# Optimization experiments

Measured on AMD Instinct MI355X. Metric: run time of the kernel, lower is better.

## Reference

```python
import jax, jax.numpy as jnp
import numpy as np

IMG = 1536
STRIDES = [8, 16, 32, 64, 128]
SCALES = np.array([2.0 ** 0, 2.0 ** (1.0 / 3.0), 2.0 ** (2.0 / 3.0)])
RATIOS = np.array([0.5, 1.0, 2.0])
THRESHOLD = 0.5
IOU_THRESHOLD = 0.5
N_KEEP = 1000  # fixed candidate budget for jit-compatible NMS


def make_anchors():
    """Multi-level RetinaNet-style anchors in (x1, y1, x2, y2), [A, 4]."""
    all_boxes = []
    for s in STRIDES:
        base = 4.0 * s
        fs = IMG // s
        areas = (base * SCALES) ** 2
        ws, hs = [], []
        for r in RATIOS:
            ws.append(np.sqrt(areas / r))
            hs.append(np.sqrt(areas * r))
        ws = np.concatenate(ws)  # [9]
        hs = np.concatenate(hs)
        cx = (np.arange(fs) + 0.5) * s
        cy = (np.arange(fs) + 0.5) * s
        cxg, cyg = np.meshgrid(cx, cy)
        cxg = cxg.reshape(-1, 1)
        cyg = cyg.reshape(-1, 1)
        boxes = np.stack([cxg - ws / 2, cyg - hs / 2, cxg + ws / 2, cyg + hs / 2], axis=-1)
        all_boxes.append(boxes.reshape(-1, 4))
    return np.concatenate(all_boxes, axis=0).astype(np.float32)


def setup_inputs() -> dict:
    key = jax.random.key(0)
    k1, k2 = jax.random.split(key)
    anchors = jnp.asarray(make_anchors())  # [441936, 4]
    A = anchors.shape[0]
    cla = jax.random.uniform(k1, (1, A, 80), dtype=jnp.float32)  # sigmoid-like class scores
    reg = 0.1 * jax.random.normal(k2, (1, A, 4), dtype=jnp.float32)  # box deltas
    return {"cla": cla, "reg": reg, "anchors": anchors, "height": IMG, "width": IMG}


def decode_box(anchors, deltas):
    wa = anchors[:, 2] - anchors[:, 0]
    ha = anchors[:, 3] - anchors[:, 1]
    cxa = anchors[:, 0] + 0.5 * wa
    cya = anchors[:, 1] + 0.5 * ha
    cx = cxa + deltas[:, 0] * wa
    cy = cya + deltas[:, 1] * ha
    w = wa * jnp.exp(deltas[:, 2])
    h = ha * jnp.exp(deltas[:, 3])
    return jnp.stack([cx - 0.5 * w, cy - 0.5 * h, cx + 0.5 * w, cy + 0.5 * h], axis=-1)


def iou_matrix(b):
    x1 = jnp.maximum(b[:, None, 0], b[None, :, 0])
    y1 = jnp.maximum(b[:, None, 1], b[None, :, 1])
    x2 = jnp.minimum(b[:, None, 2], b[None, :, 2])
    y2 = jnp.minimum(b[:, None, 3], b[None, :, 3])
    inter = jnp.clip(x2 - x1, 0.0) * jnp.clip(y2 - y1, 0.0)
    area = jnp.clip(b[:, 2] - b[:, 0], 0.0) * jnp.clip(b[:, 3] - b[:, 1], 0.0)
    union = area[:, None] + area[None, :] - inter
    return inter / jnp.maximum(union, 1e-8)


def reference(cla, reg, anchors, height, width):
    # decode + clip (clipbox)
    boxes = decode_box(anchors, reg[0])  # [A, 4]
    boxes = jnp.stack([
        jnp.clip(boxes[:, 0], 0.0, width - 1.0),
        jnp.clip(boxes[:, 1], 0.0, height - 1.0),
        jnp.clip(boxes[:, 2], 0.0, width - 1.0),
        jnp.clip(boxes[:, 3], 0.0, height - 1.0),
    ], axis=-1)
    # per-anchor best class score (torch.max over dim=2)
    scores_all = jnp.max(cla[0], axis=1)  # [A]
    # fixed-size candidate set replaces data-dependent boolean masking
    top_scores, idx = jax.lax.top_k(scores_all, N_KEEP)
    cand_boxes = boxes[idx]            # [N, 4]
    cand_cla = cla[0][idx]             # [N, C]
    valid = top_scores > THRESHOLD     # score thresholding
    iou = iou_matrix(cand_boxes)       # [N, N]

    def body(i, keep):
        suppressed = jnp.any(keep & (iou[i] > IOU_THRESHOLD))
        return keep.at[i].set(valid[i] & ~suppressed)

    keep = jax.lax.fori_loop(0, N_KEEP, body, jnp.zeros((N_KEEP,), dtype=bool))

    nms_scores = jnp.where(keep, jnp.max(cand_cla, axis=1), 0.0)
    nms_class = jnp.where(keep, jnp.argmax(cand_cla, axis=1), -1)
    nms_boxes = jnp.where(keep[:, None], cand_boxes, 0.0)
    return nms_scores, nms_class, nms_boxes
```

## Files before the change

kernel.cpp:

```cpp
#include <hip/hip_runtime.h>
#include <stdint.h>


#define NK 1000
#define CAP 2048
#define NCLS 80
#define NW 16
typedef unsigned long long ull;

static inline __device__ unsigned fkey(float f) {
  unsigned u = __float_as_uint(f);
  return (u & 0x80000000u) ? ~u : (u | 0x80000000u);
}
static inline __device__ float fkey_inv(unsigned k) {
  unsigned u = (k & 0x80000000u) ? (k & 0x7fffffffu) : ~k;
  return __uint_as_float(u);
}

__device__ __forceinline__ void scan_select(const unsigned* __restrict__ gh, int nbins,
                                            unsigned k, unsigned* s_sum, unsigned* s_res,
                                            unsigned& digit, unsigned& cum_above) {
  int t = threadIdx.x;
  int chunk = nbins >> 8;
  if (chunk < 1) chunk = 1;
  int base = t * chunk;
  unsigned s = 0;
  for (int b = 0; b < chunk; ++b) s += gh[base + b];
  s_sum[t] = s;
  __syncthreads();
  unsigned ca = 0;
  for (int u = t + 1; u < 256; ++u) ca += s_sum[u];
  if (ca < k && ca + s >= k) {
    unsigned cum = ca;
    for (int b = chunk - 1; b >= 0; --b) {
      unsigned c = gh[base + b];
      if (cum + c >= k) { s_res[0] = (unsigned)(base + b); s_res[1] = cum; break; }
      cum += c;
    }
  }
  __syncthreads();
  digit = s_res[0];
  cum_above = s_res[1];
  __syncthreads();
}

__global__ __launch_bounds__(256) void k_score(const float* __restrict__ cla,
                                               unsigned* __restrict__ keys,
                                               unsigned* __restrict__ hist0,
                                               uint4* __restrict__ zreg, int nz4,
                                               int A) {
  __shared__ unsigned lh[4096];
  int t = threadIdx.x;
  {
    const uint4 z = make_uint4(0u, 0u, 0u, 0u);
    int stride = gridDim.x * 256;
    for (int i = blockIdx.x * 256 + t; i < nz4; i += stride) zreg[i] = z;
  }
  for (int i = t; i < 4096; i += 256) lh[i] = 0u;
  __syncthreads();
  const int lane = t & 63, wib = t >> 6;
  const int gwave = blockIdx.x * 4 + wib, nwaves = gridDim.x * 4;
  const int q = lane >> 2, sub = lane & 3;
  const int ntask = (A + 15) >> 4;
  for (int task = gwave; task < ntask; task += nwaves) {
    int a = task * 16 + q;
    float m = -3.402823466e38f;
    if (a < A) {
      const float4* p = (const float4*)(cla + (size_t)a * NCLS);
#pragma unroll
      for (int j = 0; j < 5; ++j) {
        float4 v = p[sub + j * 4];
        m = fmaxf(m, fmaxf(fmaxf(v.x, v.y), fmaxf(v.z, v.w)));
      }
    }
    m = fmaxf(m, __shfl_xor(m, 1, 64));
    m = fmaxf(m, __shfl_xor(m, 2, 64));
    if (sub == 0 && a < A) {
      unsigned key = fkey(m);
      keys[a] = key;
      atomicAdd(&lh[key >> 20], 1u);
    }
  }
  __syncthreads();
  for (int i = t; i < 4096; i += 256) {
    unsigned c = lh[i];
    if (c) atomicAdd(&hist0[i], c);
  }
}

__global__ __launch_bounds__(256) void k_hist1(const unsigned* __restrict__ keys,
                                               const unsigned* __restrict__ hist0,
                                               unsigned* __restrict__ leaf,
                                               unsigned* __restrict__ summary, int A) {
  __shared__ unsigned lh[4096];
  __shared__ unsigned s_sum[256];
  __shared__ unsigned s_res[2];
  int t = threadIdx.x;
  unsigned d0, ca;
  scan_select(hist0, 4096, NK, s_sum, s_res, d0, ca);
  for (int i = t; i < 4096; i += 256) lh[i] = 0u;
  __syncthreads();
  int tid = blockIdx.x * 256 + t, nthr = gridDim.x * 256;
  for (int a = tid; a < A; a += nthr) {
    unsigned key = keys[a];
    if ((key >> 20) == d0) {
      unsigned low = key & 0xFFFFFu;
      atomicAdd(&leaf[low], 1u);
      atomicAdd(&lh[low >> 8], 1u);
    }
  }
  __syncthreads();
  for (int i = t; i < 4096; i += 256) {
    unsigned c = lh[i];
    if (c) atomicAdd(&summary[i], c);
  }
}

__global__ __launch_bounds__(256) void k_gather(const unsigned* __restrict__ keys,
                                                const unsigned* __restrict__ hist0,
                                                const unsigned* __restrict__ leaf,
                                                const unsigned* __restrict__ summary,
                                                unsigned* __restrict__ meta,
                                                ull* __restrict__ cand_keys, int A) {
  __shared__ unsigned s_sum[256];
  __shared__ unsigned s_res[2];
  __shared__ ull lbuf[1024];
  __shared__ unsigned lcnt;
  __shared__ unsigned gbase;
  int t = threadIdx.x;
  unsigned k_rem = NK, d0, g, b, ca;
  scan_select(hist0, 4096, k_rem, s_sum, s_res, d0, ca);
  k_rem -= ca;
  scan_select(summary, 4096, k_rem, s_sum, s_res, g, ca);
  k_rem -= ca;
  scan_select(leaf + (size_t)g * 256, 256, k_rem, s_sum, s_res, b, ca);
  const unsigned T = (d0 << 20) | (g << 8) | b;
  if (t == 0) lcnt = 0u;
  __syncthreads();
  int tid = blockIdx.x * 256 + t, nthr = gridDim.x * 256;
  for (int a = tid; a < A; a += nthr) {
    unsigned key = keys[a];
    if (key >= T) {
      unsigned pos = atomicAdd(&lcnt, 1u);
      if (pos < 1024)
        lbuf[pos] = ((ull)key << 32) | (ull)(~(unsigned)a);
    }
  }
  __syncthreads();
  if (t == 0) gbase = (lcnt > 0) ? atomicAdd(&meta[0], lcnt) : 0u;
  __syncthreads();
  unsigned n = lcnt < 1024u ? lcnt : 1024u;
  for (unsigned i = t; i < n; i += 256) {
    unsigned pos = gbase + i;
    if (pos < CAP) cand_keys[pos] = lbuf[i];
  }
}

__global__ __launch_bounds__(256) void k_rankdec(
    const float* __restrict__ cla, const float* __restrict__ reg,
    const float* __restrict__ anchors, const int* __restrict__ hp,
    const int* __restrict__ wp, const ull* __restrict__ cand_keys,
    float4* __restrict__ cand_box, float* __restrict__ cand_area,
    float* __restrict__ cand_score, int* __restrict__ cand_cls,
    int* __restrict__ cand_valid) {
  __shared__ ull skeys[CAP];
  int t = threadIdx.x;
  for (int i = t; i < CAP; i += 256) skeys[i] = cand_keys[i];
  __syncthreads();
  int c = blockIdx.x * 256 + t;
  ull ck = skeys[c];
  if (ck == 0ull) return;
  unsigned cnt = 0;
  const ulonglong2* sk2 = (const ulonglong2*)skeys;
#pragma unroll 4
  for (int j = 0; j < CAP / 2; ++j) {
    ulonglong2 v = sk2[j];
    cnt += (v.x > ck) ? 1u : 0u;
    cnt += (v.y > ck) ? 1u : 0u;
  }
  if (cnt >= NK) return;
  int rank = (int)cnt;
  unsigned a = ~(unsigned)(ck & 0xFFFFFFFFull);
  float score = fkey_inv((unsigned)(ck >> 32));
  float W1 = (float)wp[0] - 1.0f;
  float H1 = (float)hp[0] - 1.0f;
  float4 dd = ((const float4*)reg)[a];
  float4 an = ((const float4*)anchors)[a];
  float wa = an.z - an.x, ha = an.w - an.y;
  float cxa = an.x + 0.5f * wa, cya = an.y + 0.5f * ha;
  float cx = cxa + dd.x * wa, cy = cya + dd.y * ha;
  float w = wa * expf(dd.z), h = ha * expf(dd.w);
  float x1 = fminf(fmaxf(cx - 0.5f * w, 0.0f), W1);
  float y1 = fminf(fmaxf(cy - 0.5f * h, 0.0f), H1);
  float x2 = fminf(fmaxf(cx + 0.5f * w, 0.0f), W1);
  float y2 = fminf(fmaxf(cy + 0.5f * h, 0.0f), H1);
  cand_box[rank] = make_float4(x1, y1, x2, y2);
  cand_area[rank] = fmaxf(x2 - x1, 0.0f) * fmaxf(y2 - y1, 0.0f);
  cand_score[rank] = score;
  cand_valid[rank] = (score > 0.5f) ? 1 : 0;
  const float* row = cla + (size_t)a * NCLS;
  float m = -3.402823466e38f;
  int ci = 0;
#pragma unroll
  for (int j = 0; j < NCLS; ++j) {
    float v = row[j];
    if (v > m) { m = v; ci = j; }
  }
  cand_cls[rank] = ci;
}

__global__ __launch_bounds__(256) void k_supres(const float4* __restrict__ cand_box,
                                                const float* __restrict__ cand_area,
                                                const int* __restrict__ cand_valid,
                                                const float* __restrict__ cand_score,
                                                const int* __restrict__ cand_cls,
                                                ull* __restrict__ sup,
                                                unsigned* __restrict__ meta,
                                                float* __restrict__ out) {
  __shared__ float4 bx[NK];
  __shared__ float ar[NK];
  __shared__ ull keep_sh[NW];
  __shared__ int s_last;
  int t = threadIdx.x;
  for (int i = t; i < NK; i += 256) {
    bx[i] = cand_box[i];
    ar[i] = cand_area[i];
  }
  __syncthreads();
  int gidx = blockIdx.x * 256 + t;
  int i = gidx >> 4, w = gidx & 15;
  if (i < NK) {
    float4 bi = bx[i];
    float ai = ar[i];
    ull bits = 0ull;
    int j0 = w * 64;
    int jend = (j0 + 64 < NK) ? (j0 + 64) : NK;
    for (int j = j0; j < jend; ++j) {
      float4 bj = bx[j];
      float xx1 = fmaxf(bi.x, bj.x), yy1 = fmaxf(bi.y, bj.y);
      float xx2 = fminf(bi.z, bj.z), yy2 = fminf(bi.w, bj.w);
      float inter = fmaxf(xx2 - xx1, 0.0f) * fmaxf(yy2 - yy1, 0.0f);
      float uni = ai + ar[j] - inter;
      float iou = inter / fmaxf(uni, 1e-8f);
      if (iou > 0.5f) bits |= (1ull << (j - j0));
    }
    sup[(size_t)i * NW + w] = bits;
  }
  __threadfence();
  __syncthreads();
  if (t == 0) {
    unsigned done = __hip_atomic_fetch_add(&meta[1], 1u, __ATOMIC_ACQ_REL,
                                           __HIP_MEMORY_SCOPE_AGENT);
    s_last = (done == gridDim.x - 1) ? 1 : 0;
  }
  __syncthreads();
  if (!s_last) return;
  __threadfence();
  if (t < 64) {
    int lane = t;
    ull keepw[NW];
#pragma unroll
    for (int c = 0; c < NW; ++c) {
      int row = c * 64 + lane;
      ull rw[NW];
      int vld = 0;
      if (row < NK) {
#pragma unroll
        for (int w2 = 0; w2 < NW; ++w2)
          rw[w2] = __hip_atomic_load(&sup[(size_t)row * NW + w2], __ATOMIC_RELAXED,
                                     __HIP_MEMORY_SCOPE_AGENT);
        vld = cand_valid[row];
      } else {
#pragma unroll
        for (int w2 = 0; w2 < NW; ++w2) rw[w2] = 0ull;
      }
      ull prev = 0ull;
#pragma unroll
      for (int w2 = 0; w2 < NW; ++w2)
        if (w2 < c) prev |= rw[w2] & keepw[w2];
      int flags = (vld ? 2 : 0) | ((prev != 0ull) ? 1 : 0);
      unsigned Llo = (unsigned)rw[c];
      unsigned Lhi = (unsigned)(rw[c] >> 32);
      ull kept = 0ull;
      for (int b = 0; b < 64; ++b) {
        int fb = __shfl(flags, b, 64);
        unsigned lo = (unsigned)__shfl((int)Llo, b, 64);
        unsigned hi = (unsigned)__shfl((int)Lhi, b, 64);
        ull Lb = ((ull)hi << 32) | (ull)lo;
        bool kp = ((fb & 2) != 0) && ((fb & 1) == 0) && ((Lb & kept) == 0ull);
        kept |= ((ull)(kp ? 1u : 0u)) << b;
      }
      keepw[c] = kept;
    }
    if (lane == 0) {
#pragma unroll
      for (int w2 = 0; w2 < NW; ++w2) keep_sh[w2] = keepw[w2];
    }
  }
  __syncthreads();
  for (int i2 = t; i2 < NK; i2 += 256) {
    bool kp = (keep_sh[i2 >> 6] >> (i2 & 63)) & 1ull;
    out[i2] = kp ? cand_score[i2] : 0.0f;
    out[NK + i2] = kp ? (float)cand_cls[i2] : -1.0f;
    float4 bo = cand_box[i2];
    ((float4*)(out + 2 * NK))[i2] = kp ? bo : make_float4(0.f, 0.f, 0.f, 0.f);
  }
}

extern "C" void kernel_launch(void* const* d_in, const int* in_sizes, int n_in,
                              void* d_out, int out_size, void* d_ws, size_t ws_size,
                              hipStream_t stream) {
  const float* cla = (const float*)d_in[0];
  const float* reg = (const float*)d_in[1];
  const float* anchors = (const float*)d_in[2];
  const int* hp = (const int*)d_in[3];
  const int* wp = (const int*)d_in[4];
  float* out = (float*)d_out;
  int A = in_sizes[2] / 4;

  char* ws = (char*)d_ws;
  size_t off = 0;
  auto carve = [&](size_t bytes) -> void* {
    void* p = ws + off;
    off += bytes;
    off = (off + 255) & ~(size_t)255;
    return p;
  };
  unsigned* keys = (unsigned*)carve((size_t)A * 4);
  unsigned* hist0 = (unsigned*)carve(4096 * 4);
  char* zbase = ws + off;
  unsigned* leaf = (unsigned*)carve((size_t)(1 << 20) * 4);
  unsigned* summary = (unsigned*)carve(4096 * 4);
  unsigned* meta = (unsigned*)carve(2 * 4);
  ull* cand_keys = (ull*)carve(CAP * 8);
  size_t zbytes = (size_t)((ws + off) - zbase);
  int nz4 = (int)(zbytes / 16);
  float4* cand_box = (float4*)carve(1024 * 16);
  float* cand_area = (float*)carve(1024 * 4);
  float* cand_score = (float*)carve(1024 * 4);
  int* cand_cls = (int*)carve(1024 * 4);
  int* cand_valid = (int*)carve(1024 * 4);
  ull* sup = (ull*)carve((size_t)1024 * NW * 8);
  (void)ws_size;
  (void)n_in;
  (void)out_size;

  hipMemsetAsync(hist0, 0, 4096 * 4, stream);
  k_score<<<1024, 256, 0, stream>>>(cla, keys, hist0, (uint4*)zbase, nz4, A);
  k_hist1<<<512, 256, 0, stream>>>(keys, hist0, leaf, summary, A);
  k_gather<<<512, 256, 0, stream>>>(keys, hist0, leaf, summary, meta, cand_keys, A);
  k_rankdec<<<8, 256, 0, stream>>>(cla, reg, anchors, hp, wp, cand_keys, cand_box,
                                   cand_area, cand_score, cand_cls, cand_valid);
  k_supres<<<63, 256, 0, stream>>>(cand_box, cand_area, cand_valid, cand_score,
                                   cand_cls, sup, meta, out);
}
```

Measured before the change: 379.0 us.

## Replace serial NMS scan with parallel fixed-point resolution and triangular IoU

```diff
diff --git a/kernel.cpp b/kernel.cpp
--- a/kernel.cpp
+++ b/kernel.cpp
@@ -209,42 +209,51 @@
   cand_cls[rank] = ci;
 }
 
-__global__ __launch_bounds__(256) void k_supres(const float4* __restrict__ cand_box,
-                                                const float* __restrict__ cand_area,
-                                                const int* __restrict__ cand_valid,
-                                                const float* __restrict__ cand_score,
-                                                const int* __restrict__ cand_cls,
-                                                ull* __restrict__ sup,
-                                                unsigned* __restrict__ meta,
-                                                float* __restrict__ out) {
+__global__ __launch_bounds__(1024) void k_supres(const float4* __restrict__ cand_box,
+                                                 const float* __restrict__ cand_area,
+                                                 const int* __restrict__ cand_valid,
+                                                 const float* __restrict__ cand_score,
+                                                 const int* __restrict__ cand_cls,
+                                                 ull* __restrict__ sup,
+                                                 unsigned* __restrict__ meta,
+                                                 float* __restrict__ out) {
   __shared__ float4 bx[NK];
   __shared__ float ar[NK];
-  __shared__ ull keep_sh[NW];
+  __shared__ unsigned keptm[32], notm[32];
+  __shared__ int s_chg;
   __shared__ int s_last;
   int t = threadIdx.x;
-  for (int i = t; i < NK; i += 256) {
+  for (int i = t; i < NK; i += 1024) {
     bx[i] = cand_box[i];
     ar[i] = cand_area[i];
   }
   __syncthreads();
-  int gidx = blockIdx.x * 256 + t;
-  int i = gidx >> 4, w = gidx & 15;
-  if (i < NK) {
-    float4 bi = bx[i];
-    float ai = ar[i];
-    ull bits = 0ull;
+  {
+    int gidx = blockIdx.x * 1024 + t;
+    int i = gidx >> 4, w = gidx & 15;
     int j0 = w * 64;
-    int jend = (j0 + 64 < NK) ? (j0 + 64) : NK;
-    for (int j = j0; j < jend; ++j) {
-      float4 bj = bx[j];
-      float xx1 = fmaxf(bi.x, bj.x), yy1 = fmaxf(bi.y, bj.y);
-      float xx2 = fminf(bi.z, bj.z), yy2 = fminf(bi.w, bj.w);
-      float inter = fmaxf(xx2 - xx1, 0.0f) * fmaxf(yy2 - yy1, 0.0f);
-      float uni = ai + ar[j] - inter;
-      float iou = inter / fmaxf(uni, 1e-8f);
-      if (iou > 0.5f) bits |= (1ull << (j - j0));
-    }
-    sup[(size_t)i * NW + w] = bits;
+    if (i < NK) {
+      ull bits = 0ull;
+      if (j0 <= i) {
+        float4 bi = bx[i];
+        float ai = ar[i];
+#pragma unroll 4
+        for (int s = 0; s < 64; ++s) {
+          int jj = (s + w) & 63;
+          int j = j0 + jj;
+          if (j < NK) {
+            float4 bj = bx[j];
+            float xx1 = fmaxf(bi.x, bj.x), yy1 = fmaxf(bi.y, bj.y);
+            float xx2 = fminf(bi.z, bj.z), yy2 = fminf(bi.w, bj.w);
+            float inter = fmaxf(xx2 - xx1, 0.0f) * fmaxf(yy2 - yy1, 0.0f);
+            float uni = ai + ar[j] - inter;
+            float iou = inter / fmaxf(uni, 1e-8f);
+            if (iou > 0.5f) bits |= (1ull << jj);
+          }
+        }
+      }
+      sup[(size_t)i * NW + w] = bits;
+    }
   }
   __threadfence();
   __syncthreads();
@@ -252,57 +261,62 @@
     unsigned done = __hip_atomic_fetch_add(&meta[1], 1u, __ATOMIC_ACQ_REL,
                                            __HIP_MEMORY_SCOPE_AGENT);
     s_last = (done == gridDim.x - 1) ? 1 : 0;
+    s_chg = 0;
   }
   __syncthreads();
   if (!s_last) return;
-  __threadfence();
-  if (t < 64) {
-    int lane = t;
-    ull keepw[NW];
-#pragma unroll
-    for (int c = 0; c < NW; ++c) {
-      int row = c * 64 + lane;
-      ull rw[NW];
-      int vld = 0;
-      if (row < NK) {
-#pragma unroll
-        for (int w2 = 0; w2 < NW; ++w2)
-          rw[w2] = __hip_atomic_load(&sup[(size_t)row * NW + w2], __ATOMIC_RELAXED,
-                                     __HIP_MEMORY_SCOPE_AGENT);
-        vld = cand_valid[row];
-      } else {
-#pragma unroll
-        for (int w2 = 0; w2 < NW; ++w2) rw[w2] = 0ull;
+  if (t < 32) { keptm[t] = 0u; notm[t] = 0u; }
+  int i = t;
+  bool active = (i < NK);
+  int wi = i >> 6;
+  ull rw[NW];
+  bool decided = true;
+  if (active) {
+#pragma unroll
+    for (int w = 0; w < NW; ++w)
+      rw[w] = __hip_atomic_load(&sup[(size_t)i * NW + w], __ATOMIC_RELAXED,
+                                __HIP_MEMORY_SCOPE_AGENT);
+    int bi = i & 63;
+    ull dmask = (bi == 0) ? 0ull : ((1ull << bi) - 1ull);
+#pragma unroll
+    for (int w = 0; w < NW; ++w)
+      rw[w] = (w < wi) ? rw[w] : ((w == wi) ? (rw[w] & dmask) : 0ull);
+    decided = (cand_valid[i] == 0);
+  }
+  __syncthreads();
+  if (active && decided) atomicOr(&notm[i >> 5], 1u << (i & 31));
+  __syncthreads();
+  for (int round = 0; round < NK; ++round) {
+    if (active && !decided) {
+      ull hit = 0ull, pot = 0ull;
+#pragma unroll
+      for (int w = 0; w < NW; ++w) {
+        ull km = ((ull)keptm[2 * w + 1] << 32) | (ull)keptm[2 * w];
+        ull nm = ((ull)notm[2 * w + 1] << 32) | (ull)notm[2 * w];
+        hit |= rw[w] & km;
+        pot |= rw[w] & ~(km | nm);
       }
-      ull prev = 0ull;
-#pragma unroll
-      for (int w2 = 0; w2 < NW; ++w2)
-        if (w2 < c) prev |= rw[w2] & keepw[w2];
-      int flags = (vld ? 2 : 0) | ((prev != 0ull) ? 1 : 0);
-      unsigned Llo = (unsigned)rw[c];
-      unsigned Lhi = (unsigned)(rw[c] >> 32);
-      ull kept = 0ull;
-      for (int b = 0; b < 64; ++b) {
-        int fb = __shfl(flags, b, 64);
-        unsigned lo = (unsigned)__shfl((int)Llo, b, 64);
-        unsigned hi = (unsigned)__shfl((int)Lhi, b, 64);
-        ull Lb = ((ull)hi << 32) | (ull)lo;
-        bool kp = ((fb & 2) != 0) && ((fb & 1) == 0) && ((Lb & kept) == 0ull);
-        kept |= ((ull)(kp ? 1u : 0u)) << b;
+      if (hit) {
+        decided = true;
+        atomicOr(&notm[i >> 5], 1u << (i & 31));
+        s_chg = 1;
+      } else if (!pot) {
+        decided = true;
+        atomicOr(&keptm[i >> 5], 1u << (i & 31));
+        s_chg = 1;
       }
-      keepw[c] = kept;
-    }
-    if (lane == 0) {
-#pragma unroll
-      for (int w2 = 0; w2 < NW; ++w2) keep_sh[w2] = keepw[w2];
-    }
-  }
-  __syncthreads();
-  for (int i2 = t; i2 < NK; i2 += 256) {
-    bool kp = (keep_sh[i2 >> 6] >> (i2 & 63)) & 1ull;
+    }
+    __syncthreads();
+    if (s_chg == 0) break;
+    __syncthreads();
+    if (t == 0) s_chg = 0;
+    __syncthreads();
+  }
+  for (int i2 = t; i2 < NK; i2 += 1024) {
+    bool kp = (keptm[i2 >> 5] >> (i2 & 31)) & 1u;
     out[i2] = kp ? cand_score[i2] : 0.0f;
     out[NK + i2] = kp ? (float)cand_cls[i2] : -1.0f;
-    float4 bo = cand_box[i2];
+    float4 bo = bx[i2];
     ((float4*)(out + 2 * NK))[i2] = kp ? bo : make_float4(0.f, 0.f, 0.f, 0.f);
   }
 }
@@ -351,6 +365,6 @@
   k_gather<<<512, 256, 0, stream>>>(keys, hist0, leaf, summary, meta, cand_keys, A);
   k_rankdec<<<8, 256, 0, stream>>>(cla, reg, anchors, hp, wp, cand_keys, cand_box,
                                    cand_area, cand_score, cand_cls, cand_valid);
-  k_supres<<<63, 256, 0, stream>>>(cand_box, cand_area, cand_valid, cand_score,
-                                   cand_cls, sup, meta, out);
-}
+  k_supres<<<16, 1024, 0, stream>>>(cand_box, cand_area, cand_valid, cand_score,
+                                    cand_cls, sup, meta, out);
+}
```

Result: faster. 329.3 us (-13.1%).
